# Optimization experiments

Hardware: AMD Instinct MI355X
Metric: run time of the kernel (lower is better)

The kernel has to match this reference:

```python
import jax, jax.numpy as jnp
import numpy as np

B, H, W = 16, 768, 1024


def quat_to_rot(q):
    # q = [x, y, z, w]
    q = q / jnp.linalg.norm(q)
    x, y, z, w = q[0], q[1], q[2], q[3]
    return jnp.array([
        [1 - 2 * (y * y + z * z), 2 * (x * y - z * w), 2 * (x * z + y * w)],
        [2 * (x * y + z * w), 1 - 2 * (x * x + z * z), 2 * (y * z - x * w)],
        [2 * (x * z - y * w), 2 * (y * z + x * w), 1 - 2 * (x * x + y * y)],
    ], dtype=q.dtype)


def setup_inputs() -> dict:
    key = jax.random.key(0)
    k1, k2, k3, k4 = jax.random.split(key, 4)
    d = jax.random.uniform(k1, (B, 1, H, W), dtype=jnp.float32) * 10.0 + 0.5
    hole = jax.random.uniform(k2, (B, 1, H, W)) < 0.2
    pred = jnp.where(hole, 0.0, d)
    # small inter-frame motion so reprojections mostly land in-frame
    pos = jax.random.normal(k3, (B, 3), dtype=jnp.float32) * 0.05
    quat = jax.random.normal(k4, (B, 4), dtype=jnp.float32) * 0.05 + jnp.array([0., 0., 0., 1.])
    quat = quat / jnp.linalg.norm(quat, axis=1, keepdims=True)
    pose = jnp.concatenate([pos, quat], axis=1)
    fx = fy = 600.0
    K = jnp.array([[fx, 0., W / 2.], [0., fy, H / 2.], [0., 0., 1.]], dtype=jnp.float32)
    return {"pred": pred, "pose": pose, "K": K}


def _pair_loss(depthA, depthB, poseA, poseB, K):
    # depthA/depthB: [H, W]; poseX: [7] (xyz, quat xyzw); K: [3, 3]
    fx, fy, cx, cy = K[0, 0], K[1, 1], K[0, 2], K[1, 2]
    vs, us = jnp.meshgrid(jnp.arange(H, dtype=depthA.dtype),
                          jnp.arange(W, dtype=depthA.dtype), indexing='ij')
    validA = (depthA != 0).reshape(-1)  # pcA[pcA==0]=nan -> filtered points
    # unproject depth A to camera-frame cloud [H*W, 3]
    x = (us - cx) * depthA / fx
    y = (vs - cy) * depthA / fy
    pc = jnp.stack([x, y, depthA], axis=-1).reshape(-1, 3)
    RA, tA = quat_to_rot(poseA[3:]), poseA[:3]
    RB, tB = quat_to_rot(poseB[3:]), poseB[:3]
    pw = pc @ RA.T + tA            # world frame
    q = (pw - tB) @ RB             # camera-B frame
    z = q[:, 2]
    u2 = fx * q[:, 0] / z + cx
    v2 = fy * q[:, 1] / z + cy
    ui = jnp.round(u2).astype(jnp.int32)
    vi = jnp.round(v2).astype(jnp.int32)
    valid = validA & (z > 0) & (ui >= 0) & (ui < W) & (vi >= 0) & (vi < H)
    ui = jnp.where(valid, ui, -1)
    vi = jnp.where(valid, vi, -1)
    zz = jnp.where(valid, z, jnp.inf)
    # scatter-min reprojected depths into image B (deterministic z-buffer write)
    buf = jnp.full((H, W), jnp.inf, dtype=depthA.dtype).at[vi, ui].min(zz, mode='drop')
    hit = jnp.isfinite(buf)
    repro = jnp.where(hit, buf, depthB)  # clone of pcB overwritten at hit pixels
    diff = repro - depthB
    mask = repro != 0
    cnt = jnp.maximum(mask.sum(), 1).astype(diff.dtype)
    return jnp.sum(jnp.where(mask, diff, 0.0)) / cnt


def reference(pred, pose, K):
    dA, dB = pred[:-1, 0], pred[1:, 0]
    pA, pB = pose[:-1], pose[1:]
    losses = jax.vmap(_pair_loss, in_axes=(0, 0, 0, 0, None))(dA, dB, pA, pB, K)
    return jnp.sum(losses)
```

## Files before the change

kernel.cpp:

```cpp
#include <hip/hip_runtime.h>

#define H_ 768
#define W_ 1024
#define HW_ (H_ * W_)
#define NFRAMES 16
#define NPAIRS 15
#define NB_ 96
#define BAND_ROWS 8
#define BAND_PX (BAND_ROWS * W_)
#define ROWS_PER_BLK 4
#define BLKS_PER_PAIR (H_ / ROWS_PER_BLK)

struct Xform {
    float R[9];
    float t[3];
};

__device__ __forceinline__ bool project_px(
    float d, int u, int v,
    float fx, float fy, float cx, float cy,
    const Xform& XA, const Xform& XB,
    int& vi, int& ui, unsigned& zbits)
{
    if (d == 0.f) return false;
    float x = ((float)u - cx) * d / fx;
    float y = ((float)v - cy) * d / fy;
    float pwx = __fmaf_rn(XA.R[0], x, __fmaf_rn(XA.R[1], y, __fmaf_rn(XA.R[2], d, XA.t[0])));
    float pwy = __fmaf_rn(XA.R[3], x, __fmaf_rn(XA.R[4], y, __fmaf_rn(XA.R[5], d, XA.t[1])));
    float pwz = __fmaf_rn(XA.R[6], x, __fmaf_rn(XA.R[7], y, __fmaf_rn(XA.R[8], d, XA.t[2])));
    float mx = pwx - XB.t[0];
    float my = pwy - XB.t[1];
    float mz = pwz - XB.t[2];
    float q0 = __fmaf_rn(XB.R[0], mx, __fmaf_rn(XB.R[3], my, XB.R[6] * mz));
    float q1 = __fmaf_rn(XB.R[1], mx, __fmaf_rn(XB.R[4], my, XB.R[7] * mz));
    float z  = __fmaf_rn(XB.R[2], mx, __fmaf_rn(XB.R[5], my, XB.R[8] * mz));
    if (!(z > 0.f)) return false;
    float tu = fx * q0;
    float tv = fy * q1;
    float u2 = tu / z + cx;
    float v2 = tv / z + cy;
    int uii = (int)rintf(u2);
    int vii = (int)rintf(v2);
    if (uii < 0 || uii >= W_ || vii < 0 || vii >= H_) return false;
    vi = vii; ui = uii; zbits = __float_as_uint(z);
    return true;
}

__global__ void prep_kernel(const float* __restrict__ pose,
                            Xform* __restrict__ xf,
                            unsigned* __restrict__ hist) {
    int t = threadIdx.x;
    if (t < NFRAMES) {
        const float* p = pose + t * 7;
        float tx = p[0], ty = p[1], tz = p[2];
        float x = p[3], y = p[4], z = p[5], w = p[6];
        float n = sqrtf(x * x + y * y + z * z + w * w);
        x /= n; y /= n; z /= n; w /= n;
        Xform X;
        X.R[0] = 1.f - 2.f * (y * y + z * z);
        X.R[1] = 2.f * (x * y - z * w);
        X.R[2] = 2.f * (x * z + y * w);
        X.R[3] = 2.f * (x * y + z * w);
        X.R[4] = 1.f - 2.f * (x * x + z * z);
        X.R[5] = 2.f * (y * z - x * w);
        X.R[6] = 2.f * (x * z - y * w);
        X.R[7] = 2.f * (y * z + x * w);
        X.R[8] = 1.f - 2.f * (x * x + y * y);
        X.t[0] = tx; X.t[1] = ty; X.t[2] = tz;
        xf[t] = X;
    }
    for (int i = t; i < NPAIRS * NB_; i += 256) hist[i] = 0u;
}

__global__ void count_kernel(const float* __restrict__ pred,
                             const Xform* __restrict__ xf,
                             const float* __restrict__ Km,
                             unsigned* __restrict__ hist, int pair0) {
    int pair = pair0 + blockIdx.x / BLKS_PER_PAIR;
    int rowblk = blockIdx.x % BLKS_PER_PAIR;
    int t = threadIdx.x;
    __shared__ unsigned cnt[NB_];
    if (t < NB_) cnt[t] = 0u;
    __syncthreads();
    float fx = Km[0], cx = Km[2], fy = Km[4], cy = Km[5];
    Xform XA = xf[pair], XB = xf[pair + 1];
    int row = rowblk * ROWS_PER_BLK + (t >> 6);
    int px0 = (t & 63) * 16;
    const float* src = pred + (size_t)pair * HW_ + row * W_ + px0;
#pragma unroll
    for (int k = 0; k < 4; ++k) {
        float4 d4 = *(const float4*)(src + 4 * k);
        float dd[4] = {d4.x, d4.y, d4.z, d4.w};
#pragma unroll
        for (int j = 0; j < 4; ++j) {
            int vi, ui; unsigned zb;
            if (project_px(dd[j], px0 + 4 * k + j, row, fx, fy, cx, cy, XA, XB, vi, ui, zb))
                atomicAdd(&cnt[vi >> 3], 1u);
        }
    }
    __syncthreads();
    if (t < NB_ && cnt[t]) atomicAdd(&hist[pair * NB_ + t], cnt[t]);
}

__global__ void scan_kernel(const unsigned* __restrict__ hist,
                            unsigned* __restrict__ offsets,
                            unsigned* __restrict__ cursor,
                            int base, int n) {
    int t = threadIdx.x;
    __shared__ unsigned part[256];
    unsigned v[6];
    unsigned sum = 0;
#pragma unroll
    for (int j = 0; j < 6; ++j) {
        int i = t * 6 + j;
        v[j] = (i < n) ? hist[base + i] : 0u;
        sum += v[j];
    }
    part[t] = sum;
    __syncthreads();
    if (t == 0) {
        unsigned run = 0;
        for (int i = 0; i < 256; ++i) { unsigned tmp = part[i]; part[i] = run; run += tmp; }
        offsets[base + n] = run;
    }
    __syncthreads();
    unsigned off = part[t];
#pragma unroll
    for (int j = 0; j < 6; ++j) {
        int i = t * 6 + j;
        if (i < n) { offsets[base + i] = off; cursor[base + i] = off; off += v[j]; }
    }
}

__global__ void fill_kernel(const float* __restrict__ pred,
                            const Xform* __restrict__ xf,
                            const float* __restrict__ Km,
                            unsigned* __restrict__ cursor,
                            unsigned* __restrict__ bins, int pair0) {
    int pair = pair0 + blockIdx.x / BLKS_PER_PAIR;
    int rowblk = blockIdx.x % BLKS_PER_PAIR;
    int t = threadIdx.x;
    __shared__ unsigned cnt[NB_];
    __shared__ unsigned base[NB_];
    if (t < NB_) cnt[t] = 0u;
    __syncthreads();
    float fx = Km[0], cx = Km[2], fy = Km[4], cy = Km[5];
    Xform XA = xf[pair], XB = xf[pair + 1];
    int row = rowblk * ROWS_PER_BLK + (t >> 6);
    int px0 = (t & 63) * 16;
    const float* src = pred + (size_t)pair * HW_ + row * W_ + px0;
    unsigned pack[16];
#pragma unroll
    for (int k = 0; k < 4; ++k) {
        float4 d4 = *(const float4*)(src + 4 * k);
        float dd[4] = {d4.x, d4.y, d4.z, d4.w};
#pragma unroll
        for (int j = 0; j < 4; ++j) {
            int idx = 4 * k + j;
            pack[idx] = 0xFFFFFFFFu;
            int vi, ui; unsigned zb;
            if (project_px(dd[j], px0 + idx, row, fx, fy, cx, cy, XA, XB, vi, ui, zb)) {
                unsigned b = (unsigned)(vi >> 3);
                unsigned loc = atomicAdd(&cnt[b], 1u);
                pack[idx] = (b << 16) | loc;
            }
        }
    }
    __syncthreads();
    if (t < NB_ && cnt[t]) base[t] = atomicAdd(&cursor[pair * NB_ + t], cnt[t]);
    __syncthreads();
    int pixrow = row * W_ + px0;
#pragma unroll
    for (int idx = 0; idx < 16; ++idx) {
        unsigned pk = pack[idx];
        if (pk != 0xFFFFFFFFu)
            bins[base[pk >> 16] + (pk & 0xFFFFu)] = (unsigned)(pixrow + idx);
    }
}

__global__ void zmin_kernel(const float* __restrict__ pred,
                            const Xform* __restrict__ xf,
                            const float* __restrict__ Km,
                            const unsigned* __restrict__ offsets,
                            const unsigned* __restrict__ bins,
                            float* __restrict__ partial_s,
                            unsigned* __restrict__ partial_c, int pair0) {
    int gband = pair0 * NB_ + blockIdx.x;
    int pair = gband / NB_;
    int band = gband % NB_;
    int t = threadIdx.x;
    __shared__ unsigned zb[BAND_PX];
#pragma unroll
    for (int k = 0; k < BAND_PX / 256; ++k) zb[k * 256 + t] = 0xFFFFFFFFu;
    __syncthreads();
    float fx = Km[0], cx = Km[2], fy = Km[4], cy = Km[5];
    Xform XA = xf[pair], XB = xf[pair + 1];
    unsigned off0 = offsets[gband], off1 = offsets[gband + 1];
    const float* predA = pred + (size_t)pair * HW_;
    for (unsigned i = off0 + t; i < off1; i += 256) {
        unsigned pix = bins[i];
        float d = predA[pix];
        int vi, ui; unsigned zbits;
        if (project_px(d, (int)(pix & (W_ - 1)), (int)(pix >> 10),
                       fx, fy, cx, cy, XA, XB, vi, ui, zbits))
            atomicMin(&zb[((vi & (BAND_ROWS - 1)) << 10) | ui], zbits);
    }
    __syncthreads();
    const float4* pb4 = (const float4*)(pred + (size_t)(pair + 1) * HW_ + (size_t)band * BAND_PX);
    const uint4* zb4 = (const uint4*)zb;
    float s = 0.f; unsigned c = 0u;
#pragma unroll
    for (int k = 0; k < BAND_PX / 1024; ++k) {
        int i4 = k * 256 + t;
        uint4 b = zb4[i4];
        float4 db = pb4[i4];
        if (b.x != 0xFFFFFFFFu) { s += __uint_as_float(b.x) - db.x; ++c; } else if (db.x != 0.f) ++c;
        if (b.y != 0xFFFFFFFFu) { s += __uint_as_float(b.y) - db.y; ++c; } else if (db.y != 0.f) ++c;
        if (b.z != 0xFFFFFFFFu) { s += __uint_as_float(b.z) - db.z; ++c; } else if (db.z != 0.f) ++c;
        if (b.w != 0xFFFFFFFFu) { s += __uint_as_float(b.w) - db.w; ++c; } else if (db.w != 0.f) ++c;
    }
    for (int off = 32; off > 0; off >>= 1) {
        s += __shfl_down(s, off);
        c += __shfl_down(c, off);
    }
    __shared__ float ls[4];
    __shared__ unsigned lc[4];
    int lane = t & 63, wid = t >> 6;
    if (lane == 0) { ls[wid] = s; lc[wid] = c; }
    __syncthreads();
    if (t == 0) {
        partial_s[gband] = ls[0] + ls[1] + ls[2] + ls[3];
        partial_c[gband] = lc[0] + lc[1] + lc[2] + lc[3];
    }
}

__global__ void final_kernel(const float* __restrict__ partial_s,
                             const unsigned* __restrict__ partial_c,
                             float* __restrict__ out) {
    int t = threadIdx.x;
    __shared__ float ps[NPAIRS];
    __shared__ unsigned pc[NPAIRS];
    int pair = t >> 4, sub = t & 15;
    float s = 0.f; unsigned c = 0u;
    if (t < NPAIRS * 16) {
#pragma unroll
        for (int j = 0; j < 6; ++j) {
            int g = pair * NB_ + sub + j * 16;
            s += partial_s[g];
            c += partial_c[g];
        }
        for (int m = 1; m < 16; m <<= 1) { s += __shfl_xor(s, m); c += __shfl_xor(c, m); }
        if (sub == 0) { ps[pair] = s; pc[pair] = c; }
    }
    __syncthreads();
    if (t == 0) {
        float acc = 0.f;
        for (int p = 0; p < NPAIRS; ++p) {
            unsigned cc = pc[p];
            if (cc < 1u) cc = 1u;
            acc += ps[p] / (float)cc;
        }
        out[0] = acc;
    }
}

extern "C" void kernel_launch(void* const* d_in, const int* in_sizes, int n_in,
                              void* d_out, int out_size, void* d_ws, size_t ws_size,
                              hipStream_t stream) {
    const float* pred = (const float*)d_in[0];
    const float* pose = (const float*)d_in[1];
    const float* Km   = (const float*)d_in[2];
    float* out = (float*)d_out;
    char* ws = (char*)d_ws;

    unsigned* hist      = (unsigned*)ws;
    unsigned* offsets   = hist + NPAIRS * NB_;
    unsigned* cursor    = offsets + NPAIRS * NB_ + 1;
    unsigned* partial_c = cursor + NPAIRS * NB_;
    float*    partial_s = (float*)(partial_c + NPAIRS * NB_);
    Xform*    xf        = (Xform*)(ws + 28864);
    unsigned* bins      = (unsigned*)(ws + 29696);

    size_t binsA = (size_t)NPAIRS * HW_ * sizeof(unsigned);
    bool pathA = ws_size >= 29696 + binsA;

    prep_kernel<<<1, 256, 0, stream>>>(pose, xf, hist);

    if (pathA) {
        count_kernel<<<NPAIRS * BLKS_PER_PAIR, 256, 0, stream>>>(pred, xf, Km, hist, 0);
        scan_kernel<<<1, 256, 0, stream>>>(hist, offsets, cursor, 0, NPAIRS * NB_);
        fill_kernel<<<NPAIRS * BLKS_PER_PAIR, 256, 0, stream>>>(pred, xf, Km, cursor, bins, 0);
        zmin_kernel<<<NPAIRS * NB_, 256, 0, stream>>>(pred, xf, Km, offsets, bins,
                                                      partial_s, partial_c, 0);
    } else {
        for (int p = 0; p < NPAIRS; ++p) {
            count_kernel<<<BLKS_PER_PAIR, 256, 0, stream>>>(pred, xf, Km, hist, p);
            scan_kernel<<<1, 256, 0, stream>>>(hist, offsets, cursor, p * NB_, NB_);
            fill_kernel<<<BLKS_PER_PAIR, 256, 0, stream>>>(pred, xf, Km, cursor, bins, p);
            zmin_kernel<<<NB_, 256, 0, stream>>>(pred, xf, Km, offsets, bins,
                                                 partial_s, partial_c, p);
        }
    }

    final_kernel<<<1, 256, 0, stream>>>(partial_s, partial_c, out);
}
```

Measured before the change: 200.0 us.

## Replace count/scan binning with segment allocation and packed quantized depth entries

Removes the count and scan passes. Each fill block now reserves a contiguous chunk with one global atomic and records per-band segments (base, count), so the binning runs in a single projection pass. Bins store a packed entry of quantized depth (upper 19 bits, rounded) plus the in-band slot, so zmin no longer re-reads depth or re-projects pixels, and its atomicMin works directly on the packed value. In exchange, depth loses its low 13 mantissa bits, which changes the loss values slightly. It also adds a segment table with fixed capacity per band and more scattered reads in zmin.

```diff
diff --git a/kernel.cpp b/kernel.cpp
--- a/kernel.cpp
+++ b/kernel.cpp
@@ -10,6 +10,8 @@
 #define BAND_PX (BAND_ROWS * W_)
 #define ROWS_PER_BLK 4
 #define BLKS_PER_PAIR (H_ / ROWS_PER_BLK)
+#define MAXSEG BLKS_PER_PAIR
+#define NBANDS_ALL (NPAIRS * NB_)
 
 struct Xform {
     float R[9];
@@ -35,10 +37,8 @@
     float q1 = __fmaf_rn(XB.R[1], mx, __fmaf_rn(XB.R[4], my, XB.R[7] * mz));
     float z  = __fmaf_rn(XB.R[2], mx, __fmaf_rn(XB.R[5], my, XB.R[8] * mz));
     if (!(z > 0.f)) return false;
-    float tu = fx * q0;
-    float tv = fy * q1;
-    float u2 = tu / z + cx;
-    float v2 = tv / z + cy;
+    float u2 = fx * q0 / z + cx;
+    float v2 = fy * q1 / z + cy;
     int uii = (int)rintf(u2);
     int vii = (int)rintf(v2);
     if (uii < 0 || uii >= W_ || vii < 0 || vii >= H_) return false;
@@ -48,7 +48,8 @@
 
 __global__ void prep_kernel(const float* __restrict__ pose,
                             Xform* __restrict__ xf,
-                            unsigned* __restrict__ hist) {
+                            unsigned* __restrict__ seg_cnt,
+                            unsigned* __restrict__ alloc) {
     int t = threadIdx.x;
     if (t < NFRAMES) {
         const float* p = pose + t * 7;
@@ -69,119 +70,83 @@
         X.t[0] = tx; X.t[1] = ty; X.t[2] = tz;
         xf[t] = X;
     }
-    for (int i = t; i < NPAIRS * NB_; i += 256) hist[i] = 0u;
-}
-
-__global__ void count_kernel(const float* __restrict__ pred,
-                             const Xform* __restrict__ xf,
-                             const float* __restrict__ Km,
-                             unsigned* __restrict__ hist, int pair0) {
+    for (int i = t; i < NBANDS_ALL; i += 256) seg_cnt[i] = 0u;
+    if (t == 0) alloc[0] = 0u;
+}
+
+__global__ void reset_alloc_kernel(unsigned* __restrict__ alloc) {
+    alloc[0] = 0u;
+}
+
+__global__ void fill_kernel(const float* __restrict__ pred,
+                            const Xform* __restrict__ xf,
+                            const float* __restrict__ Km,
+                            unsigned* __restrict__ alloc,
+                            unsigned* __restrict__ seg_cnt,
+                            uint2* __restrict__ seg,
+                            unsigned* __restrict__ bins, int pair0) {
     int pair = pair0 + blockIdx.x / BLKS_PER_PAIR;
     int rowblk = blockIdx.x % BLKS_PER_PAIR;
     int t = threadIdx.x;
     __shared__ unsigned cnt[NB_];
+    __shared__ unsigned basev[NB_];
+    __shared__ unsigned chunk_base;
     if (t < NB_) cnt[t] = 0u;
     __syncthreads();
+
     float fx = Km[0], cx = Km[2], fy = Km[4], cy = Km[5];
     Xform XA = xf[pair], XB = xf[pair + 1];
     int row = rowblk * ROWS_PER_BLK + (t >> 6);
     int px0 = (t & 63) * 16;
     const float* src = pred + (size_t)pair * HW_ + row * W_ + px0;
+
+    unsigned entry[16];
+    unsigned pk[16];
 #pragma unroll
     for (int k = 0; k < 4; ++k) {
         float4 d4 = *(const float4*)(src + 4 * k);
         float dd[4] = {d4.x, d4.y, d4.z, d4.w};
 #pragma unroll
         for (int j = 0; j < 4; ++j) {
-            int vi, ui; unsigned zb;
-            if (project_px(dd[j], px0 + 4 * k + j, row, fx, fy, cx, cy, XA, XB, vi, ui, zb))
-                atomicAdd(&cnt[vi >> 3], 1u);
-        }
-    }
-    __syncthreads();
-    if (t < NB_ && cnt[t]) atomicAdd(&hist[pair * NB_ + t], cnt[t]);
-}
-
-__global__ void scan_kernel(const unsigned* __restrict__ hist,
-                            unsigned* __restrict__ offsets,
-                            unsigned* __restrict__ cursor,
-                            int base, int n) {
-    int t = threadIdx.x;
-    __shared__ unsigned part[256];
-    unsigned v[6];
-    unsigned sum = 0;
-#pragma unroll
-    for (int j = 0; j < 6; ++j) {
-        int i = t * 6 + j;
-        v[j] = (i < n) ? hist[base + i] : 0u;
-        sum += v[j];
-    }
-    part[t] = sum;
+            int idx = 4 * k + j;
+            pk[idx] = 0xFFFFFFFFu;
+            int vi, ui; unsigned zbits;
+            if (project_px(dd[j], px0 + idx, row, fx, fy, cx, cy, XA, XB, vi, ui, zbits)) {
+                unsigned band = (unsigned)(vi >> 3);
+                unsigned slot = (((unsigned)vi & 7u) << 10) | (unsigned)ui;
+                unsigned zq = (zbits + 0x1000u) >> 13;
+                entry[idx] = (zq << 13) | slot;
+                unsigned loc = atomicAdd(&cnt[band], 1u);
+                pk[idx] = (band << 16) | loc;
+            }
+        }
+    }
     __syncthreads();
     if (t == 0) {
         unsigned run = 0;
-        for (int i = 0; i < 256; ++i) { unsigned tmp = part[i]; part[i] = run; run += tmp; }
-        offsets[base + n] = run;
-    }
-    __syncthreads();
-    unsigned off = part[t];
-#pragma unroll
-    for (int j = 0; j < 6; ++j) {
-        int i = t * 6 + j;
-        if (i < n) { offsets[base + i] = off; cursor[base + i] = off; off += v[j]; }
-    }
-}
-
-__global__ void fill_kernel(const float* __restrict__ pred,
-                            const Xform* __restrict__ xf,
-                            const float* __restrict__ Km,
-                            unsigned* __restrict__ cursor,
-                            unsigned* __restrict__ bins, int pair0) {
-    int pair = pair0 + blockIdx.x / BLKS_PER_PAIR;
-    int rowblk = blockIdx.x % BLKS_PER_PAIR;
-    int t = threadIdx.x;
-    __shared__ unsigned cnt[NB_];
-    __shared__ unsigned base[NB_];
-    if (t < NB_) cnt[t] = 0u;
-    __syncthreads();
-    float fx = Km[0], cx = Km[2], fy = Km[4], cy = Km[5];
-    Xform XA = xf[pair], XB = xf[pair + 1];
-    int row = rowblk * ROWS_PER_BLK + (t >> 6);
-    int px0 = (t & 63) * 16;
-    const float* src = pred + (size_t)pair * HW_ + row * W_ + px0;
-    unsigned pack[16];
-#pragma unroll
-    for (int k = 0; k < 4; ++k) {
-        float4 d4 = *(const float4*)(src + 4 * k);
-        float dd[4] = {d4.x, d4.y, d4.z, d4.w};
-#pragma unroll
-        for (int j = 0; j < 4; ++j) {
-            int idx = 4 * k + j;
-            pack[idx] = 0xFFFFFFFFu;
-            int vi, ui; unsigned zb;
-            if (project_px(dd[j], px0 + idx, row, fx, fy, cx, cy, XA, XB, vi, ui, zb)) {
-                unsigned b = (unsigned)(vi >> 3);
-                unsigned loc = atomicAdd(&cnt[b], 1u);
-                pack[idx] = (b << 16) | loc;
-            }
-        }
-    }
-    __syncthreads();
-    if (t < NB_ && cnt[t]) base[t] = atomicAdd(&cursor[pair * NB_ + t], cnt[t]);
-    __syncthreads();
-    int pixrow = row * W_ + px0;
+        for (int i = 0; i < NB_; ++i) { unsigned c = cnt[i]; basev[i] = run; run += c; }
+        chunk_base = atomicAdd(alloc, run);
+    }
+    __syncthreads();
+    if (t < NB_ && cnt[t]) {
+        unsigned b0 = chunk_base + basev[t];
+        basev[t] = b0;
+        unsigned gb = (unsigned)(pair * NB_ + t);
+        unsigned si = atomicAdd(&seg_cnt[gb], 1u);
+        seg[(size_t)gb * MAXSEG + si] = make_uint2(b0, cnt[t]);
+    }
+    __syncthreads();
 #pragma unroll
     for (int idx = 0; idx < 16; ++idx) {
-        unsigned pk = pack[idx];
-        if (pk != 0xFFFFFFFFu)
-            bins[base[pk >> 16] + (pk & 0xFFFFu)] = (unsigned)(pixrow + idx);
+        unsigned p = pk[idx];
+        if (p != 0xFFFFFFFFu)
+            bins[basev[p >> 16] + (p & 0xFFFFu)] = entry[idx];
     }
 }
 
 __global__ void zmin_kernel(const float* __restrict__ pred,
-                            const Xform* __restrict__ xf,
-                            const float* __restrict__ Km,
-                            const unsigned* __restrict__ offsets,
+                            const unsigned* __restrict__ seg_cnt,
+                            const uint2* __restrict__ seg,
                             const unsigned* __restrict__ bins,
                             float* __restrict__ partial_s,
                             unsigned* __restrict__ partial_c, int pair0) {
@@ -193,19 +158,18 @@
 #pragma unroll
     for (int k = 0; k < BAND_PX / 256; ++k) zb[k * 256 + t] = 0xFFFFFFFFu;
     __syncthreads();
-    float fx = Km[0], cx = Km[2], fy = Km[4], cy = Km[5];
-    Xform XA = xf[pair], XB = xf[pair + 1];
-    unsigned off0 = offsets[gband], off1 = offsets[gband + 1];
-    const float* predA = pred + (size_t)pair * HW_;
-    for (unsigned i = off0 + t; i < off1; i += 256) {
-        unsigned pix = bins[i];
-        float d = predA[pix];
-        int vi, ui; unsigned zbits;
-        if (project_px(d, (int)(pix & (W_ - 1)), (int)(pix >> 10),
-                       fx, fy, cx, cy, XA, XB, vi, ui, zbits))
-            atomicMin(&zb[((vi & (BAND_ROWS - 1)) << 10) | ui], zbits);
-    }
-    __syncthreads();
+
+    unsigned ns = seg_cnt[gband];
+    const uint2* sgs = seg + (size_t)gband * MAXSEG;
+    for (unsigned j = 0; j < ns; ++j) {
+        uint2 sg = sgs[j];
+        for (unsigned i = sg.x + t; i < sg.x + sg.y; i += 256) {
+            unsigned e = bins[i];
+            atomicMin(&zb[e & 8191u], e >> 13);
+        }
+    }
+    __syncthreads();
+
     const float4* pb4 = (const float4*)(pred + (size_t)(pair + 1) * HW_ + (size_t)band * BAND_PX);
     const uint4* zb4 = (const uint4*)zb;
     float s = 0.f; unsigned c = 0u;
@@ -214,10 +178,10 @@
         int i4 = k * 256 + t;
         uint4 b = zb4[i4];
         float4 db = pb4[i4];
-        if (b.x != 0xFFFFFFFFu) { s += __uint_as_float(b.x) - db.x; ++c; } else if (db.x != 0.f) ++c;
-        if (b.y != 0xFFFFFFFFu) { s += __uint_as_float(b.y) - db.y; ++c; } else if (db.y != 0.f) ++c;
-        if (b.z != 0xFFFFFFFFu) { s += __uint_as_float(b.z) - db.z; ++c; } else if (db.z != 0.f) ++c;
-        if (b.w != 0xFFFFFFFFu) { s += __uint_as_float(b.w) - db.w; ++c; } else if (db.w != 0.f) ++c;
+        if (b.x != 0xFFFFFFFFu) { s += __uint_as_float(b.x << 13) - db.x; ++c; } else if (db.x != 0.f) ++c;
+        if (b.y != 0xFFFFFFFFu) { s += __uint_as_float(b.y << 13) - db.y; ++c; } else if (db.y != 0.f) ++c;
+        if (b.z != 0xFFFFFFFFu) { s += __uint_as_float(b.z << 13) - db.z; ++c; } else if (db.z != 0.f) ++c;
+        if (b.w != 0xFFFFFFFFu) { s += __uint_as_float(b.w << 13) - db.w; ++c; } else if (db.w != 0.f) ++c;
     }
     for (int off = 32; off > 0; off >>= 1) {
         s += __shfl_down(s, off);
@@ -273,31 +237,30 @@
     float* out = (float*)d_out;
     char* ws = (char*)d_ws;
 
-    unsigned* hist      = (unsigned*)ws;
-    unsigned* offsets   = hist + NPAIRS * NB_;
-    unsigned* cursor    = offsets + NPAIRS * NB_ + 1;
-    unsigned* partial_c = cursor + NPAIRS * NB_;
-    float*    partial_s = (float*)(partial_c + NPAIRS * NB_);
-    Xform*    xf        = (Xform*)(ws + 28864);
-    unsigned* bins      = (unsigned*)(ws + 29696);
-
-    size_t binsA = (size_t)NPAIRS * HW_ * sizeof(unsigned);
-    bool pathA = ws_size >= 29696 + binsA;
-
-    prep_kernel<<<1, 256, 0, stream>>>(pose, xf, hist);
+    unsigned* seg_cnt   = (unsigned*)ws;
+    unsigned* alloc     = (unsigned*)(ws + 5760);
+    unsigned* partial_c = (unsigned*)(ws + 5764);
+    float*    partial_s = (float*)(ws + 11524);
+    Xform*    xf        = (Xform*)(ws + 17296);
+    uint2*    seg       = (uint2*)(ws + 18064);
+    unsigned* bins      = (unsigned*)(ws + 2229904);
+
+    size_t needA = 2229904 + (size_t)NPAIRS * HW_ * sizeof(unsigned);
+    bool pathA = ws_size >= needA;
+
+    prep_kernel<<<1, 256, 0, stream>>>(pose, xf, seg_cnt, alloc);
 
     if (pathA) {
-        count_kernel<<<NPAIRS * BLKS_PER_PAIR, 256, 0, stream>>>(pred, xf, Km, hist, 0);
-        scan_kernel<<<1, 256, 0, stream>>>(hist, offsets, cursor, 0, NPAIRS * NB_);
-        fill_kernel<<<NPAIRS * BLKS_PER_PAIR, 256, 0, stream>>>(pred, xf, Km, cursor, bins, 0);
-        zmin_kernel<<<NPAIRS * NB_, 256, 0, stream>>>(pred, xf, Km, offsets, bins,
+        fill_kernel<<<NPAIRS * BLKS_PER_PAIR, 256, 0, stream>>>(pred, xf, Km, alloc,
+                                                                seg_cnt, seg, bins, 0);
+        zmin_kernel<<<NPAIRS * NB_, 256, 0, stream>>>(pred, seg_cnt, seg, bins,
                                                       partial_s, partial_c, 0);
     } else {
         for (int p = 0; p < NPAIRS; ++p) {
-            count_kernel<<<BLKS_PER_PAIR, 256, 0, stream>>>(pred, xf, Km, hist, p);
-            scan_kernel<<<1, 256, 0, stream>>>(hist, offsets, cursor, p * NB_, NB_);
-            fill_kernel<<<BLKS_PER_PAIR, 256, 0, stream>>>(pred, xf, Km, cursor, bins, p);
-            zmin_kernel<<<NB_, 256, 0, stream>>>(pred, xf, Km, offsets, bins,
+            reset_alloc_kernel<<<1, 1, 0, stream>>>(alloc);
+            fill_kernel<<<BLKS_PER_PAIR, 256, 0, stream>>>(pred, xf, Km, alloc,
+                                                           seg_cnt, seg, bins, p);
+            zmin_kernel<<<NB_, 256, 0, stream>>>(pred, seg_cnt, seg, bins,
                                                  partial_s, partial_c, p);
         }
     }
```

New measurement: 173.3 us. 13.3% less time.
